# Kernel optimization log

Hardware: AMD Instinct MI355X
Metric: run time of the kernel (lower is better)

Reference implementation:

```python
import jax, jax.numpy as jnp
import numpy as np

# dims mirroring the torch module: dim=32 (MVN), omega=8, d_head=n_embd//n_head
B, T, E, DH = 8, 2048, 1024, 32
OMEGA, DIM = 8, 32
M = OMEGA * DIM  # 256 random features (omega concatenated N(0, I_dim) samples)


def setup_inputs() -> dict:
    key = jax.random.key(0)
    ks = jax.random.split(key, 8)
    s = 1.0 / np.sqrt(E).astype(np.float32)  # torch Linear-like init scale
    return {
        "x": jax.random.normal(ks[0], (B, T, E), jnp.float32),
        "Wq": jax.random.normal(ks[1], (E, DH), jnp.float32) * s,
        "bq": jax.random.normal(ks[2], (DH,), jnp.float32) * s,
        "Wk": jax.random.normal(ks[3], (E, DH), jnp.float32) * s,
        "bk": jax.random.normal(ks[4], (DH,), jnp.float32) * s,
        "Wv": jax.random.normal(ks[5], (E, DH), jnp.float32) * s,
        "bv": jax.random.normal(ks[6], (DH,), jnp.float32) * s,
        # random-feature matrix: omega stacked samples from N(0, I_DIM) -> [M, DH]
        "w": jax.random.normal(ks[7], (M, DH), jnp.float32),
    }


def reference(x, Wq, bq, Wk, bk, Wv, bv, w):
    # projections (as in Head.forward)
    q = x @ Wq + bq  # [B,T,DH]
    k = x @ Wk + bk  # [B,T,DH]
    v = x @ Wv + bv  # computed but unused, exactly as in the source
    del v
    # Aprox_softmax (FAVOR+-style hyperbolic random features), vectorized per token
    z = k + q                                          # [B,T,DH]
    zsqr = jnp.sum(k * k, -1) + jnp.sum(q * q, -1)     # [B,T]  (per-token norms)
    A = jnp.exp(-0.5 * zsqr)                           # [B,T]
    cosH = jnp.cosh(jnp.einsum('btd,md->btm', z, w))   # [B,T,M]
    R = A[..., None] * cosH                            # [B,T,M]
    return R
```

## Files before the change

### kernel.cpp

```cpp
#include <hip/hip_runtime.h>
#include <cstdint>

#define E_DIM   1024
#define DH      32
#define M_FEAT  256
#define BT      16384

typedef __attribute__((ext_vector_type(8))) short bf16x8;
typedef __attribute__((ext_vector_type(4))) float f32x4;

#define WP_H_OFF 0
#define WP_L_OFF 65536

__device__ __forceinline__ unsigned perm_hi2(unsigned lo_src, unsigned hi_src) {
#if __has_builtin(__builtin_amdgcn_perm)
    return __builtin_amdgcn_perm(hi_src, lo_src, 0x07060302u);
#else
    return (lo_src >> 16) | (hi_src & 0xFFFF0000u);
#endif
}

__device__ __forceinline__ void split2(float f0, float f1, unsigned& ph, unsigned& pl) {
    unsigned u0 = __builtin_bit_cast(unsigned, f0);
    unsigned u1 = __builtin_bit_cast(unsigned, f1);
    ph = perm_hi2(u0, u1);
    float d0 = f0 - __builtin_bit_cast(float, u0 & 0xFFFF0000u);
    float d1 = f1 - __builtin_bit_cast(float, u1 & 0xFFFF0000u);
    pl = perm_hi2(__builtin_bit_cast(unsigned, d0), __builtin_bit_cast(unsigned, d1));
}

__device__ __forceinline__ void split8(const float4& a, const float4& b,
                                       uint4& uh, uint4& ul) {
    split2(a.x, a.y, uh.x, ul.x);
    split2(a.z, a.w, uh.y, ul.y);
    split2(b.x, b.y, uh.z, ul.z);
    split2(b.z, b.w, uh.w, ul.w);
}

__global__ __launch_bounds__(256) void k_prep(
    const float* __restrict__ Wq, const float* __restrict__ Wk,
    short* __restrict__ ws)
{
    __shared__ float wlds[128 * 36];
    const int b = blockIdx.x, tid = threadIdx.x;
    const float* __restrict__ src = (b < 8) ? Wq : Wk;
    const int k0 = (b & 7) * 128;
    const int nbase = (b < 8) ? 0 : 32;
#pragma unroll
    for (int it = 0; it < 4; ++it) {
        int f = it * 256 + tid;
        int k = f >> 3, c4 = f & 7;
        float4 v = *(const float4*)(src + (size_t)(k0 + k) * DH + c4 * 4);
        *(float4*)&wlds[k * 36 + c4 * 4] = v;
    }
    __syncthreads();
    const int n = tid >> 3, kq = tid & 7;
    const int n_g = nbase + n;
    const int nt = n_g >> 4, ln = n_g & 15;
#pragma unroll
    for (int rep = 0; rep < 4; ++rep) {
        int kk = rep * 8 + kq;
        int k_g = k0 + kk * 4;
        float f0 = wlds[(kk * 4 + 0) * 36 + n];
        float f1 = wlds[(kk * 4 + 1) * 36 + n];
        float f2 = wlds[(kk * 4 + 2) * 36 + n];
        float f3 = wlds[(kk * 4 + 3) * 36 + n];
        uint2 ph, pl;
        split2(f0, f1, ph.x, pl.x);
        split2(f2, f3, ph.y, pl.y);
        int sub = k_g >> 5;
        int g = (k_g >> 3) & 3, j0 = k_g & 7;
        int lane = g * 16 + ln;
        size_t flat = ((size_t)(nt * 32 + sub)) * 512 + lane * 8 + j0;
        *(uint2*)(ws + WP_H_OFF + flat) = ph;
        *(uint2*)(ws + WP_L_OFF + flat) = pl;
    }
}

#define TB 16
#define XS2 136
#define QS 68
#define ZS 40

__global__ __launch_bounds__(256, 4) void k_main(
    const float* __restrict__ x, const float* __restrict__ bq,
    const float* __restrict__ bk, const short* __restrict__ ws,
    const float* __restrict__ w, float* __restrict__ out)
{
    __shared__ __align__(16) short xh_s[2][TB * XS2];
    __shared__ __align__(16) short xl_s[2][TB * XS2];
    __shared__ __align__(16) float qk_f[TB * QS];
    __shared__ __align__(16) short zh_s[TB * ZS];
    __shared__ __align__(16) short zl_s[TB * ZS];
    __shared__ float lnA_f[TB];

    const int tid  = threadIdx.x;
    const int lane = tid & 63;
    const int wv   = __builtin_amdgcn_readfirstlane(tid >> 6);
    const int ln15 = lane & 15;
    const int g    = lane >> 4;
    const long t0  = (long)blockIdx.x * TB;

    const int nrow = wv * 16 + ln15;
    const float bias = (nrow < 32) ? bq[nrow] : bk[nrow - 32];

    const int kq = tid & 15;
    const int mr = tid >> 4;

    f32x4 acc = {0.f, 0.f, 0.f, 0.f};

    const short* wpB_h = ws + WP_H_OFF + (size_t)(wv * 32) * 512 + lane * 8;
    const short* wpB_l = ws + WP_L_OFF + (size_t)(wv * 32) * 512 + lane * 8;
    const float* xrow  = x + (t0 + mr) * E_DIM + kq * 8;

    float4 st[16];
#pragma unroll
    for (int p = 0; p < 8; ++p) {
        st[2 * p]     = *(const float4*)(xrow + p * 128);
        st[2 * p + 1] = *(const float4*)(xrow + p * 128 + 4);
    }
    {
        uint4 uh, ul;
        split8(st[0], st[1], uh, ul);
        *(uint4*)&xh_s[0][mr * XS2 + kq * 8] = uh;
        *(uint4*)&xl_s[0][mr * XS2 + kq * 8] = ul;
    }

#pragma unroll
    for (int p = 0; p < 8; ++p) {
        __syncthreads();
        bf16x8 bh[4], bl[4];
#pragma unroll
        for (int j = 0; j < 4; ++j) {
            bh[j] = *(const bf16x8*)(wpB_h + (size_t)(p * 4 + j) * 512);
            bl[j] = *(const bf16x8*)(wpB_l + (size_t)(p * 4 + j) * 512);
        }
#pragma unroll
        for (int j = 0; j < 4; ++j) {
            bf16x8 ah = *(const bf16x8*)&xh_s[p & 1][ln15 * XS2 + j * 32 + g * 8];
            bf16x8 al = *(const bf16x8*)&xl_s[p & 1][ln15 * XS2 + j * 32 + g * 8];
            acc = __builtin_amdgcn_mfma_f32_16x16x32_bf16(ah, bh[j], acc, 0, 0, 0);
            acc = __builtin_amdgcn_mfma_f32_16x16x32_bf16(ah, bl[j], acc, 0, 0, 0);
            acc = __builtin_amdgcn_mfma_f32_16x16x32_bf16(al, bh[j], acc, 0, 0, 0);
        }
        if (p < 7) {
            uint4 uh, ul;
            split8(st[2 * p + 2], st[2 * p + 3], uh, ul);
            *(uint4*)&xh_s[(p + 1) & 1][mr * XS2 + kq * 8] = uh;
            *(uint4*)&xl_s[(p + 1) & 1][mr * XS2 + kq * 8] = ul;
        }
    }

    float4 wfa[4], wfb[4];
#pragma unroll
    for (int i = 0; i < 4; ++i) {
        const int nf = (wv * 4 + i) * 16 + ln15;
        wfa[i] = *(const float4*)(w + (size_t)nf * DH + g * 8);
        wfb[i] = *(const float4*)(w + (size_t)nf * DH + g * 8 + 4);
    }

#pragma unroll
    for (int r = 0; r < 4; ++r)
        qk_f[(g * 4 + r) * QS + nrow] = acc[r] + bias;
    __syncthreads();

    if (tid < 128) {
        const int tok = tid >> 3, grp = tid & 7;
        float4 qv = *(const float4*)&qk_f[tok * QS + grp * 4];
        float4 kv = *(const float4*)&qk_f[tok * QS + 32 + grp * 4];
        float z0 = qv.x + kv.x, z1 = qv.y + kv.y, z2 = qv.z + kv.z, z3 = qv.w + kv.w;
        float p = qv.x*qv.x + qv.y*qv.y + qv.z*qv.z + qv.w*qv.w
                + kv.x*kv.x + kv.y*kv.y + kv.z*kv.z + kv.w*kv.w;
        uint2 ph, pl;
        split2(z0, z1, ph.x, pl.x);
        split2(z2, z3, ph.y, pl.y);
        *(uint2*)&zh_s[tok * ZS + grp * 4] = ph;
        *(uint2*)&zl_s[tok * ZS + grp * 4] = pl;
        p += __shfl_xor(p, 1);
        p += __shfl_xor(p, 2);
        p += __shfl_xor(p, 4);
        if (grp == 0) lnA_f[tok] = -0.5f * p;
    }
    __syncthreads();

    f32x4 facc[4];
#pragma unroll
    for (int i = 0; i < 4; ++i) facc[i] = (f32x4){0.f,0.f,0.f,0.f};

    bf16x8 a_h = *(const bf16x8*)&zh_s[ln15 * ZS + g * 8];
    bf16x8 a_l = *(const bf16x8*)&zl_s[ln15 * ZS + g * 8];
#pragma unroll
    for (int i = 0; i < 4; ++i) {
        uint4 uh, ul;
        split8(wfa[i], wfb[i], uh, ul);
        bf16x8 wh = __builtin_bit_cast(bf16x8, uh);
        bf16x8 wl = __builtin_bit_cast(bf16x8, ul);
        facc[i] = __builtin_amdgcn_mfma_f32_16x16x32_bf16(a_h, wh, facc[i], 0, 0, 0);
        facc[i] = __builtin_amdgcn_mfma_f32_16x16x32_bf16(a_h, wl, facc[i], 0, 0, 0);
        facc[i] = __builtin_amdgcn_mfma_f32_16x16x32_bf16(a_l, wh, facc[i], 0, 0, 0);
    }

    float lnAv[4];
#pragma unroll
    for (int r = 0; r < 4; ++r) lnAv[r] = lnA_f[g * 4 + r];

#pragma unroll
    for (int i = 0; i < 4; ++i) {
        const int n = (wv * 4 + i) * 16 + ln15;
#pragma unroll
        for (int r = 0; r < 4; ++r) {
            float s = facc[i][r];
            float R = 0.5f * (__expf(lnAv[r] + s) + __expf(lnAv[r] - s));
            out[(t0 + g * 4 + r) * M_FEAT + n] = R;
        }
    }
}

extern "C" void kernel_launch(void* const* d_in, const int* in_sizes, int n_in,
                              void* d_out, int out_size, void* d_ws, size_t ws_size,
                              hipStream_t stream) {
    const float* x  = (const float*)d_in[0];
    const float* Wq = (const float*)d_in[1];
    const float* bq = (const float*)d_in[2];
    const float* Wk = (const float*)d_in[3];
    const float* bk = (const float*)d_in[4];
    const float* w  = (const float*)d_in[7];
    float* out = (float*)d_out;
    short* ws  = (short*)d_ws;

    k_prep<<<dim3(16), dim3(256), 0, stream>>>(Wq, Wk, ws);
    k_main<<<dim3(BT / TB), dim3(256), 0, stream>>>(x, bq, bk, ws, w, out);
}
```

Baseline: 123.9 us.

## Double token tile per block and stream x loads per stage

Each main-kernel block now handles 32 tokens instead of 16, so every weight fragment loaded from global memory feeds two MFMA row tiles. The full up-front register prefetch of x is replaced by a one-stage-ahead load inside the pipelined loop, cutting register use. Occupancy hint drops from 4 to 3 blocks per CU, and the prep kernel is split across 32 smaller blocks. The risk is fewer resident blocks and less latency hiding for the x loads, since only one stage is prefetched.

```diff
diff --git a/kernel.cpp b/kernel.cpp
--- a/kernel.cpp
+++ b/kernel.cpp
@@ -41,13 +41,13 @@
     const float* __restrict__ Wq, const float* __restrict__ Wk,
     short* __restrict__ ws)
 {
-    __shared__ float wlds[128 * 36];
+    __shared__ float wlds[64 * 36];
     const int b = blockIdx.x, tid = threadIdx.x;
-    const float* __restrict__ src = (b < 8) ? Wq : Wk;
-    const int k0 = (b & 7) * 128;
-    const int nbase = (b < 8) ? 0 : 32;
-#pragma unroll
-    for (int it = 0; it < 4; ++it) {
+    const float* __restrict__ src = (b < 16) ? Wq : Wk;
+    const int k0 = (b & 15) * 64;
+    const int nbase = (b < 16) ? 0 : 32;
+#pragma unroll
+    for (int it = 0; it < 2; ++it) {
         int f = it * 256 + tid;
         int k = f >> 3, c4 = f & 7;
         float4 v = *(const float4*)(src + (size_t)(k0 + k) * DH + c4 * 4);
@@ -58,7 +58,7 @@
     const int n_g = nbase + n;
     const int nt = n_g >> 4, ln = n_g & 15;
 #pragma unroll
-    for (int rep = 0; rep < 4; ++rep) {
+    for (int rep = 0; rep < 2; ++rep) {
         int kk = rep * 8 + kq;
         int k_g = k0 + kk * 4;
         float f0 = wlds[(kk * 4 + 0) * 36 + n];
@@ -77,12 +77,12 @@
     }
 }
 
-#define TB 16
+#define TB 32
 #define XS2 136
 #define QS 68
 #define ZS 40
 
-__global__ __launch_bounds__(256, 4) void k_main(
+__global__ __launch_bounds__(256, 3) void k_main(
     const float* __restrict__ x, const float* __restrict__ bq,
     const float* __restrict__ bk, const short* __restrict__ ws,
     const float* __restrict__ w, float* __restrict__ out)
@@ -107,47 +107,58 @@
     const int kq = tid & 15;
     const int mr = tid >> 4;
 
-    f32x4 acc = {0.f, 0.f, 0.f, 0.f};
+    f32x4 acc0 = {0.f, 0.f, 0.f, 0.f};
+    f32x4 acc1 = {0.f, 0.f, 0.f, 0.f};
 
     const short* wpB_h = ws + WP_H_OFF + (size_t)(wv * 32) * 512 + lane * 8;
     const short* wpB_l = ws + WP_L_OFF + (size_t)(wv * 32) * 512 + lane * 8;
-    const float* xrow  = x + (t0 + mr) * E_DIM + kq * 8;
-
-    float4 st[16];
-#pragma unroll
-    for (int p = 0; p < 8; ++p) {
-        st[2 * p]     = *(const float4*)(xrow + p * 128);
-        st[2 * p + 1] = *(const float4*)(xrow + p * 128 + 4);
-    }
+    const float* xr0 = x + (t0 + mr) * (size_t)E_DIM + kq * 8;
+    const float* xr1 = x + (t0 + mr + 16) * (size_t)E_DIM + kq * 8;
+
+    float4 a0 = *(const float4*)(xr0 + 0), b0 = *(const float4*)(xr0 + 4);
+    float4 a1 = *(const float4*)(xr1 + 0), b1 = *(const float4*)(xr1 + 4);
     {
         uint4 uh, ul;
-        split8(st[0], st[1], uh, ul);
+        split8(a0, b0, uh, ul);
         *(uint4*)&xh_s[0][mr * XS2 + kq * 8] = uh;
         *(uint4*)&xl_s[0][mr * XS2 + kq * 8] = ul;
+        split8(a1, b1, uh, ul);
+        *(uint4*)&xh_s[0][(mr + 16) * XS2 + kq * 8] = uh;
+        *(uint4*)&xl_s[0][(mr + 16) * XS2 + kq * 8] = ul;
     }
 
 #pragma unroll
     for (int p = 0; p < 8; ++p) {
         __syncthreads();
-        bf16x8 bh[4], bl[4];
+        if (p < 7) {
+            a0 = *(const float4*)(xr0 + (p + 1) * 128);
+            b0 = *(const float4*)(xr0 + (p + 1) * 128 + 4);
+            a1 = *(const float4*)(xr1 + (p + 1) * 128);
+            b1 = *(const float4*)(xr1 + (p + 1) * 128 + 4);
+        }
 #pragma unroll
         for (int j = 0; j < 4; ++j) {
-            bh[j] = *(const bf16x8*)(wpB_h + (size_t)(p * 4 + j) * 512);
-            bl[j] = *(const bf16x8*)(wpB_l + (size_t)(p * 4 + j) * 512);
-        }
-#pragma unroll
-        for (int j = 0; j < 4; ++j) {
-            bf16x8 ah = *(const bf16x8*)&xh_s[p & 1][ln15 * XS2 + j * 32 + g * 8];
-            bf16x8 al = *(const bf16x8*)&xl_s[p & 1][ln15 * XS2 + j * 32 + g * 8];
-            acc = __builtin_amdgcn_mfma_f32_16x16x32_bf16(ah, bh[j], acc, 0, 0, 0);
-            acc = __builtin_amdgcn_mfma_f32_16x16x32_bf16(ah, bl[j], acc, 0, 0, 0);
-            acc = __builtin_amdgcn_mfma_f32_16x16x32_bf16(al, bh[j], acc, 0, 0, 0);
+            bf16x8 bh = *(const bf16x8*)(wpB_h + (size_t)(p * 4 + j) * 512);
+            bf16x8 bl = *(const bf16x8*)(wpB_l + (size_t)(p * 4 + j) * 512);
+            bf16x8 ah0 = *(const bf16x8*)&xh_s[p & 1][ln15 * XS2 + j * 32 + g * 8];
+            bf16x8 al0 = *(const bf16x8*)&xl_s[p & 1][ln15 * XS2 + j * 32 + g * 8];
+            bf16x8 ah1 = *(const bf16x8*)&xh_s[p & 1][(ln15 + 16) * XS2 + j * 32 + g * 8];
+            bf16x8 al1 = *(const bf16x8*)&xl_s[p & 1][(ln15 + 16) * XS2 + j * 32 + g * 8];
+            acc0 = __builtin_amdgcn_mfma_f32_16x16x32_bf16(ah0, bh, acc0, 0, 0, 0);
+            acc0 = __builtin_amdgcn_mfma_f32_16x16x32_bf16(ah0, bl, acc0, 0, 0, 0);
+            acc0 = __builtin_amdgcn_mfma_f32_16x16x32_bf16(al0, bh, acc0, 0, 0, 0);
+            acc1 = __builtin_amdgcn_mfma_f32_16x16x32_bf16(ah1, bh, acc1, 0, 0, 0);
+            acc1 = __builtin_amdgcn_mfma_f32_16x16x32_bf16(ah1, bl, acc1, 0, 0, 0);
+            acc1 = __builtin_amdgcn_mfma_f32_16x16x32_bf16(al1, bh, acc1, 0, 0, 0);
         }
         if (p < 7) {
             uint4 uh, ul;
-            split8(st[2 * p + 2], st[2 * p + 3], uh, ul);
+            split8(a0, b0, uh, ul);
             *(uint4*)&xh_s[(p + 1) & 1][mr * XS2 + kq * 8] = uh;
             *(uint4*)&xl_s[(p + 1) & 1][mr * XS2 + kq * 8] = ul;
+            split8(a1, b1, uh, ul);
+            *(uint4*)&xh_s[(p + 1) & 1][(mr + 16) * XS2 + kq * 8] = uh;
+            *(uint4*)&xl_s[(p + 1) & 1][(mr + 16) * XS2 + kq * 8] = ul;
         }
     }
 
@@ -160,11 +171,13 @@
     }
 
 #pragma unroll
-    for (int r = 0; r < 4; ++r)
-        qk_f[(g * 4 + r) * QS + nrow] = acc[r] + bias;
+    for (int r = 0; r < 4; ++r) {
+        qk_f[(g * 4 + r) * QS + nrow]        = acc0[r] + bias;
+        qk_f[(16 + g * 4 + r) * QS + nrow]   = acc1[r] + bias;
+    }
     __syncthreads();
 
-    if (tid < 128) {
+    {
         const int tok = tid >> 3, grp = tid & 7;
         float4 qv = *(const float4*)&qk_f[tok * QS + grp * 4];
         float4 kv = *(const float4*)&qk_f[tok * QS + 32 + grp * 4];
@@ -183,35 +196,49 @@
     }
     __syncthreads();
 
-    f32x4 facc[4];
-#pragma unroll
-    for (int i = 0; i < 4; ++i) facc[i] = (f32x4){0.f,0.f,0.f,0.f};
-
-    bf16x8 a_h = *(const bf16x8*)&zh_s[ln15 * ZS + g * 8];
-    bf16x8 a_l = *(const bf16x8*)&zl_s[ln15 * ZS + g * 8];
+    f32x4 facc[4][2];
+#pragma unroll
+    for (int i = 0; i < 4; ++i)
+#pragma unroll
+        for (int mt = 0; mt < 2; ++mt) facc[i][mt] = (f32x4){0.f,0.f,0.f,0.f};
+
+    bf16x8 a_h[2], a_l[2];
+#pragma unroll
+    for (int mt = 0; mt < 2; ++mt) {
+        a_h[mt] = *(const bf16x8*)&zh_s[(mt * 16 + ln15) * ZS + g * 8];
+        a_l[mt] = *(const bf16x8*)&zl_s[(mt * 16 + ln15) * ZS + g * 8];
+    }
 #pragma unroll
     for (int i = 0; i < 4; ++i) {
         uint4 uh, ul;
         split8(wfa[i], wfb[i], uh, ul);
         bf16x8 wh = __builtin_bit_cast(bf16x8, uh);
         bf16x8 wl = __builtin_bit_cast(bf16x8, ul);
-        facc[i] = __builtin_amdgcn_mfma_f32_16x16x32_bf16(a_h, wh, facc[i], 0, 0, 0);
-        facc[i] = __builtin_amdgcn_mfma_f32_16x16x32_bf16(a_h, wl, facc[i], 0, 0, 0);
-        facc[i] = __builtin_amdgcn_mfma_f32_16x16x32_bf16(a_l, wh, facc[i], 0, 0, 0);
-    }
-
-    float lnAv[4];
-#pragma unroll
-    for (int r = 0; r < 4; ++r) lnAv[r] = lnA_f[g * 4 + r];
+#pragma unroll
+        for (int mt = 0; mt < 2; ++mt) {
+            facc[i][mt] = __builtin_amdgcn_mfma_f32_16x16x32_bf16(a_h[mt], wh, facc[i][mt], 0, 0, 0);
+            facc[i][mt] = __builtin_amdgcn_mfma_f32_16x16x32_bf16(a_h[mt], wl, facc[i][mt], 0, 0, 0);
+            facc[i][mt] = __builtin_amdgcn_mfma_f32_16x16x32_bf16(a_l[mt], wh, facc[i][mt], 0, 0, 0);
+        }
+    }
+
+    float lnAv[2][4];
+#pragma unroll
+    for (int mt = 0; mt < 2; ++mt)
+#pragma unroll
+        for (int r = 0; r < 4; ++r) lnAv[mt][r] = lnA_f[mt * 16 + g * 4 + r];
 
 #pragma unroll
     for (int i = 0; i < 4; ++i) {
         const int n = (wv * 4 + i) * 16 + ln15;
 #pragma unroll
-        for (int r = 0; r < 4; ++r) {
-            float s = facc[i][r];
-            float R = 0.5f * (__expf(lnAv[r] + s) + __expf(lnAv[r] - s));
-            out[(t0 + g * 4 + r) * M_FEAT + n] = R;
+        for (int mt = 0; mt < 2; ++mt) {
+#pragma unroll
+            for (int r = 0; r < 4; ++r) {
+                float s = facc[i][mt][r];
+                float R = 0.5f * (__expf(lnAv[mt][r] + s) + __expf(lnAv[mt][r] - s));
+                out[(t0 + mt * 16 + g * 4 + r) * M_FEAT + n] = R;
+            }
         }
     }
 }
@@ -228,6 +255,6 @@
     float* out = (float*)d_out;
     short* ws  = (short*)d_ws;
 
-    k_prep<<<dim3(16), dim3(256), 0, stream>>>(Wq, Wk, ws);
+    k_prep<<<dim3(32), dim3(256), 0, stream>>>(Wq, Wk, ws);
     k_main<<<dim3(BT / TB), dim3(256), 0, stream>>>(x, bq, bk, ws, w, out);
 }
```

New measurement: 122.1 us. No clear change (-1.5%).
